# Kernel tuning notes

Hardware: AMD Instinct MI355X
Metric: run time of the kernel (lower is better)

The kernel has to match this reference:

```python
import jax, jax.numpy as jnp
import numpy as np

MORA_DIV = 2


def setup_inputs() -> dict:
    key = jax.random.key(0)
    k1, k2, k3, k4 = jax.random.split(key, 4)
    d = 4096
    m = d // MORA_DIV
    x = jax.random.normal(k1, (4, 2048, d), dtype=jnp.float32)
    weight = jax.random.normal(k2, (d, d), dtype=jnp.float32) * 0.02
    mora = jax.random.normal(k3, (m, m), dtype=jnp.float32) * 0.02
    # dora_mag initialized as column L2 norm of the frozen weight (1, d_in)
    dora_mag = jnp.linalg.norm(weight, axis=0, keepdims=True)
    return {"x": x, "weight": weight, "mora": mora, "dora_mag": dora_mag}


def reference(x, weight, mora, dora_mag):
    # Tile the small adapter into full (d_out, d_in): repeat_interleave on both dims
    adapter = jnp.repeat(jnp.repeat(mora, MORA_DIV, axis=0), MORA_DIV, axis=1)
    w = weight + adapter                      # (d_out, d_in)
    col_norm = jnp.linalg.norm(w, axis=0, keepdims=True)  # (1, d_in)
    w = dora_mag * (w / col_norm)             # DoRA magnitude rescale
    return jnp.einsum('bsd,od->bso', x, w)    # F.linear, no bias
```

## Files before the change

kernel.cpp:

```cpp
#include <hip/hip_runtime.h>
#include <stdint.h>

#define M_TOT 8192
#define N_TOT 4096
#define K_TOT 4096
#define BM 256
#define BN 256
#define BK 64
#define NIT (K_TOT / (2 * BK))

typedef short  s16x8 __attribute__((ext_vector_type(8)));
typedef unsigned short u16x8 __attribute__((ext_vector_type(8)));
typedef float  f32x4 __attribute__((ext_vector_type(4)));

__device__ __forceinline__ unsigned short f32_to_bf16(float f) {
  union { float f; unsigned u; } v; v.f = f;
  unsigned r = v.u + 0x7FFFu + ((v.u >> 16) & 1u);
  return (unsigned short)(r >> 16);
}

__device__ __forceinline__ void gload_lds16(void* lds, const void* g) {
  __builtin_amdgcn_global_load_lds(
      (const __attribute__((address_space(1))) unsigned int*)g,
      (__attribute__((address_space(3))) unsigned int*)lds,
      16, 0, 0);
}

__global__ void colnorm_partial_k(const float* __restrict__ weight,
                                  const float* __restrict__ mora,
                                  float* __restrict__ partials) {
  int d = blockIdx.x * 256 + threadIdx.x;
  int o0 = blockIdx.y * 128;
  float s = 0.f;
  #pragma unroll 4
  for (int o = o0; o < o0 + 128; ++o) {
    float w = weight[(size_t)o * K_TOT + d] + mora[(size_t)(o >> 1) * 2048 + (d >> 1)];
    s = fmaf(w, w, s);
  }
  partials[blockIdx.y * K_TOT + d] = s;
}

__global__ void scale_k(const float* __restrict__ partials,
                        const float* __restrict__ dora_mag,
                        float* __restrict__ scale) {
  int d = blockIdx.x * 256 + threadIdx.x;
  float s = 0.f;
  #pragma unroll
  for (int c = 0; c < 32; ++c) s += partials[c * K_TOT + d];
  scale[d] = dora_mag[d] / sqrtf(s);
}

__global__ void pack_w_k(const float* __restrict__ weight,
                         const float* __restrict__ mora,
                         const float* __restrict__ scale,
                         unsigned short* __restrict__ wb) {
  size_t idx = ((size_t)blockIdx.x * 256 + threadIdx.x) * 8;
  int o = (int)(idx >> 12);
  int d = (int)(idx & (K_TOT - 1));
  float4 w0 = *(const float4*)(weight + idx);
  float4 w1 = *(const float4*)(weight + idx + 4);
  float4 mv = *(const float4*)(mora + (size_t)(o >> 1) * 2048 + (d >> 1));
  float4 s0 = *(const float4*)(scale + d);
  float4 s1 = *(const float4*)(scale + d + 4);
  u16x8 r;
  r[0] = f32_to_bf16((w0.x + mv.x) * s0.x);
  r[1] = f32_to_bf16((w0.y + mv.x) * s0.y);
  r[2] = f32_to_bf16((w0.z + mv.y) * s0.z);
  r[3] = f32_to_bf16((w0.w + mv.y) * s0.w);
  r[4] = f32_to_bf16((w1.x + mv.z) * s1.x);
  r[5] = f32_to_bf16((w1.y + mv.z) * s1.y);
  r[6] = f32_to_bf16((w1.z + mv.w) * s1.z);
  r[7] = f32_to_bf16((w1.w + mv.w) * s1.w);
  *(u16x8*)(wb + idx) = r;
}

__global__ void pack_x_k(const float* __restrict__ x, unsigned short* __restrict__ xb) {
  size_t idx = ((size_t)blockIdx.x * 256 + threadIdx.x) * 8;
  float4 v0 = *(const float4*)(x + idx);
  float4 v1 = *(const float4*)(x + idx + 4);
  u16x8 r;
  r[0] = f32_to_bf16(v0.x); r[1] = f32_to_bf16(v0.y);
  r[2] = f32_to_bf16(v0.z); r[3] = f32_to_bf16(v0.w);
  r[4] = f32_to_bf16(v1.x); r[5] = f32_to_bf16(v1.y);
  r[6] = f32_to_bf16(v1.z); r[7] = f32_to_bf16(v1.w);
  *(u16x8*)(xb + idx) = r;
}

__global__ void __launch_bounds__(512, 2) gemm_bf16_k(
    const unsigned short* __restrict__ xb,
    const unsigned short* __restrict__ wb,
    float* __restrict__ out) {
  __shared__ short lds[2][2][2][128 * 64];

  const int tid = threadIdx.x;
  const int l   = tid & 63;
  const int wid = tid >> 6;
  const int wm  = wid >> 2;
  const int wn  = wid & 3;
  const int wnh = wn >> 1;

  const int orig = blockIdx.x;
  const int swz  = (orig & 7) * (512 >> 3) + (orig >> 3);
  const int by = swz >> 4;
  const int bx = swz & 15;

  const unsigned short* ag = xb + (size_t)(by * BM) * K_TOT;
  const unsigned short* bg = wb + (size_t)(bx * BN) * K_TOT;

  const int row0 = tid >> 3;
  const int kb0  = (tid & 7) ^ (row0 & 7);
  const int off0 = row0 * K_TOT + kb0 * 8;
  const int off1 = off0 + 64 * K_TOT;
  const int ldst = (tid & ~63) * 8;

  const int lrow = l & 15;
  const int lq   = l >> 4;
  const int key  = lrow & 7;
  const int ab0  = lrow * 64 + ((lq) ^ key) * 8;
  const int ab1  = lrow * 64 + ((4 + lq) ^ key) * 8;

  s16x8 aA[4][2], bB[4][2];
  f32x4 acc[8][4] = {};

#define STAGE(buf, op, h, t) { \
    short* d = &lds[buf][op][h][0] + ldst; \
    const unsigned short* s = ((op) ? bg : ag) + (size_t)(h) * 128 * K_TOT + (size_t)(t) * BK; \
    gload_lds16(d, s + off0); \
    gload_lds16(d + 4096, s + off1); }
#define DSA(buf, mh) { const short* p = &lds[buf][0][wm][0]; \
    _Pragma("unroll") for (int mm = 0; mm < 4; ++mm) { \
      aA[mm][0] = *(const s16x8*)(p + ((mh) * 4 + mm) * 1024 + ab0); \
      aA[mm][1] = *(const s16x8*)(p + ((mh) * 4 + mm) * 1024 + ab1); } }
#define DSB(buf, nh) { const short* p = &lds[buf][1][wnh][0] + (wn & 1) * 4096; \
    _Pragma("unroll") for (int nn = 0; nn < 2; ++nn) { \
      bB[(nh) * 2 + nn][0] = *(const s16x8*)(p + ((nh) * 2 + nn) * 1024 + ab0); \
      bB[(nh) * 2 + nn][1] = *(const s16x8*)(p + ((nh) * 2 + nn) * 1024 + ab1); } }
#define MMQ(mh, nh) { __builtin_amdgcn_s_setprio(1); \
    _Pragma("unroll") for (int mm = 0; mm < 4; ++mm) \
      _Pragma("unroll") for (int nn = 0; nn < 2; ++nn) \
        _Pragma("unroll") for (int kh = 0; kh < 2; ++kh) \
          acc[(mh) * 4 + mm][(nh) * 2 + nn] = __builtin_amdgcn_mfma_f32_16x16x32_bf16( \
              aA[mm][kh], bB[(nh) * 2 + nn][kh], acc[(mh) * 4 + mm][(nh) * 2 + nn], 0, 0, 0); \
    __builtin_amdgcn_s_setprio(0); }
#define BARm()  asm volatile("s_barrier" ::: "memory")
#define VM6()   asm volatile("s_waitcnt vmcnt(6)" ::: "memory")
#define VM4()   asm volatile("s_waitcnt vmcnt(4)" ::: "memory")
#define VM0()   asm volatile("s_waitcnt vmcnt(0)" ::: "memory")

  STAGE(0, 0, 0, 0); STAGE(0, 0, 1, 0); STAGE(0, 1, 0, 0); STAGE(0, 1, 1, 0);
  STAGE(1, 1, 0, 1); STAGE(1, 1, 1, 1); STAGE(1, 0, 0, 1);
  VM6(); BARm();

  #pragma unroll 1
  for (int i = 0; i < NIT - 1; ++i) {
    const int t1 = 2 * i + 1;
    const int t2 = t1 + 1;
    const int t3 = t1 + 2;
    DSA(0, 0); DSB(0, 0); STAGE(1, 0, 1, t1);
    MMQ(0, 0); BARm();
    DSB(0, 1);
    MMQ(0, 1); BARm();
    DSA(0, 1); STAGE(0, 1, 0, t2);
    MMQ(1, 0); BARm();
    STAGE(0, 1, 1, t2);
    MMQ(1, 1); VM4(); BARm();
    DSA(1, 0); DSB(1, 0); STAGE(0, 0, 0, t2);
    MMQ(0, 0); BARm();
    DSB(1, 1); STAGE(0, 0, 1, t2);
    MMQ(0, 1); BARm();
    DSA(1, 1); STAGE(1, 1, 0, t3);
    MMQ(1, 0); BARm();
    STAGE(1, 1, 1, t3); STAGE(1, 0, 0, t3);
    MMQ(1, 1); VM6(); BARm();
  }

  DSA(0, 0); DSB(0, 0); STAGE(1, 0, 1, 63);
  MMQ(0, 0); BARm();
  DSB(0, 1);
  MMQ(0, 1); BARm();
  DSA(0, 1);
  MMQ(1, 0); BARm();
  MMQ(1, 1); VM0(); BARm();
  DSA(1, 0); DSB(1, 0);
  MMQ(0, 0); BARm();
  DSB(1, 1);
  MMQ(0, 1); BARm();
  DSA(1, 1);
  MMQ(1, 0); BARm();
  MMQ(1, 1);

#undef STAGE
#undef DSA
#undef DSB
#undef MMQ

  const int row0o = by * BM + wm * 128 + lq * 4;
  const int col0o = bx * BN + wn * 64 + lrow;
  #pragma unroll
  for (int m = 0; m < 8; ++m)
    #pragma unroll
    for (int n = 0; n < 4; ++n) {
      #pragma unroll
      for (int j = 0; j < 4; ++j)
        out[(size_t)(row0o + m * 16 + j) * N_TOT + col0o + n * 16] = acc[m][n][j];
    }
}

__global__ void gemm_fb_k(const float* __restrict__ x, const float* __restrict__ weight,
                          const float* __restrict__ mora, const float* __restrict__ scale,
                          float* __restrict__ out) {
  __shared__ float As[64][17];
  __shared__ float Bs[64][17];
  int t = threadIdx.x;
  int bx = blockIdx.x, by = blockIdx.y;
  int tr = t >> 4, tc = t & 15;
  float c[4][4] = {};
  for (int kt = 0; kt < K_TOT; kt += 16) {
    #pragma unroll
    for (int r = 0; r < 4; ++r) {
      int idx = r * 256 + t;
      int row = idx >> 4, col = idx & 15;
      As[row][col] = x[(size_t)(by * 64 + row) * K_TOT + kt + col];
      int o = bx * 64 + row, d = kt + col;
      Bs[row][col] = (weight[(size_t)o * K_TOT + d] + mora[(size_t)(o >> 1) * 2048 + (d >> 1)]) * scale[d];
    }
    __syncthreads();
    #pragma unroll
    for (int k = 0; k < 16; ++k) {
      float av[4], bv[4];
      #pragma unroll
      for (int i = 0; i < 4; ++i) av[i] = As[tr * 4 + i][k];
      #pragma unroll
      for (int j = 0; j < 4; ++j) bv[j] = Bs[tc * 4 + j][k];
      #pragma unroll
      for (int i = 0; i < 4; ++i)
        #pragma unroll
        for (int j = 0; j < 4; ++j)
          c[i][j] = fmaf(av[i], bv[j], c[i][j]);
    }
    __syncthreads();
  }
  #pragma unroll
  for (int i = 0; i < 4; ++i)
    #pragma unroll
    for (int j = 0; j < 4; ++j)
      out[(size_t)(by * 64 + tr * 4 + i) * N_TOT + bx * 64 + tc * 4 + j] = c[i][j];
}

extern "C" void kernel_launch(void* const* d_in, const int* in_sizes, int n_in,
                              void* d_out, int out_size, void* d_ws, size_t ws_size,
                              hipStream_t stream) {
  const float* x      = (const float*)d_in[0];
  const float* weight = (const float*)d_in[1];
  const float* mora   = (const float*)d_in[2];
  const float* dora   = (const float*)d_in[3];
  float* out = (float*)d_out;

  char* ws = (char*)d_ws;
  float* partials = (float*)ws;
  float* scale    = (float*)(ws + (512 << 10));
  const size_t OFF_W = (size_t)1 << 20;
  unsigned short* wbuf = (unsigned short*)(ws + OFF_W);
  unsigned short* xbuf = (unsigned short*)(ws + OFF_W + (size_t)N_TOT * K_TOT * 2);
  const size_t NEED = OFF_W + (size_t)N_TOT * K_TOT * 2 + (size_t)M_TOT * K_TOT * 2;

  dim3 b256(256);
  colnorm_partial_k<<<dim3(16, 32), b256, 0, stream>>>(weight, mora, partials);
  scale_k<<<16, b256, 0, stream>>>(partials, dora, scale);

  if (ws_size >= NEED) {
    pack_w_k<<<(N_TOT * K_TOT) / (256 * 8), b256, 0, stream>>>(weight, mora, scale, wbuf);
    pack_x_k<<<(M_TOT * K_TOT) / (256 * 8), b256, 0, stream>>>(x, xbuf);
    gemm_bf16_k<<<(M_TOT / BM) * (N_TOT / BN), 512, 0, stream>>>(xbuf, wbuf, out);
  } else {
    gemm_fb_k<<<dim3(N_TOT / 64, M_TOT / 64), b256, 0, stream>>>(x, weight, mora, scale, out);
  }
}
```

Before: 303.1 us.

## Reorder GEMM main loop to issue LDS reads after MFMA quadrants

Reorders the 8-phase main loop so that each phase starts its MFMA quadrant first and then issues the next LDS fragment reads and global-to-LDS stages, instead of loading before computing. The goal is to overlap LDS read latency with matrix-core work and to shorten the dependency stalls before each MFMA block. The change also alters when register fragments are overwritten relative to their use, so correctness depends on the compiler keeping the right ordering, and register pressure may rise.

```diff
diff --git a/kernel.cpp b/kernel.cpp
--- a/kernel.cpp
+++ b/kernel.cpp
@@ -156,36 +156,22 @@
     const int t1 = 2 * i + 1;
     const int t2 = t1 + 1;
     const int t3 = t1 + 2;
-    DSA(0, 0); DSB(0, 0); STAGE(1, 0, 1, t1);
-    MMQ(0, 0); BARm();
-    DSB(0, 1);
-    MMQ(0, 1); BARm();
-    DSA(0, 1); STAGE(0, 1, 0, t2);
-    MMQ(1, 0); BARm();
-    STAGE(0, 1, 1, t2);
-    MMQ(1, 1); VM4(); BARm();
-    DSA(1, 0); DSB(1, 0); STAGE(0, 0, 0, t2);
-    MMQ(0, 0); BARm();
-    DSB(1, 1); STAGE(0, 0, 1, t2);
-    MMQ(0, 1); BARm();
-    DSA(1, 1); STAGE(1, 1, 0, t3);
-    MMQ(1, 0); BARm();
-    STAGE(1, 1, 1, t3); STAGE(1, 0, 0, t3);
-    MMQ(1, 1); VM6(); BARm();
-  }
-
-  DSA(0, 0); DSB(0, 0); STAGE(1, 0, 1, 63);
-  MMQ(0, 0); BARm();
-  DSB(0, 1);
-  MMQ(0, 1); BARm();
-  DSA(0, 1);
+    DSA(0, 0); DSB(0, 0); MMQ(0, 0); DSB(0, 1); STAGE(1, 0, 1, t1); BARm();
+    MMQ(0, 1); DSA(0, 1); BARm();
+    MMQ(1, 0); STAGE(0, 1, 0, t2); BARm();
+    MMQ(1, 1); STAGE(0, 1, 1, t2); VM4(); BARm();
+    DSA(1, 0); DSB(1, 0); MMQ(0, 0); DSB(1, 1); STAGE(0, 0, 0, t2); BARm();
+    MMQ(0, 1); DSA(1, 1); STAGE(0, 0, 1, t2); BARm();
+    MMQ(1, 0); STAGE(1, 1, 0, t3); BARm();
+    MMQ(1, 1); STAGE(1, 1, 1, t3); STAGE(1, 0, 0, t3); VM6(); BARm();
+  }
+
+  DSA(0, 0); DSB(0, 0); MMQ(0, 0); DSB(0, 1); STAGE(1, 0, 1, 63); BARm();
+  MMQ(0, 1); DSA(0, 1); BARm();
   MMQ(1, 0); BARm();
   MMQ(1, 1); VM0(); BARm();
-  DSA(1, 0); DSB(1, 0);
-  MMQ(0, 0); BARm();
-  DSB(1, 1);
-  MMQ(0, 1); BARm();
-  DSA(1, 1);
+  DSA(1, 0); DSB(1, 0); MMQ(0, 0); DSB(1, 1); BARm();
+  MMQ(0, 1); DSA(1, 1); BARm();
   MMQ(1, 0); BARm();
   MMQ(1, 1);
 
```

Measured after the change: 298.8 us (median of 2 runs). No clear change (-1.4%).
